# Performance work log

Measured on AMD Instinct MI355X. Metric: run time of the kernel, lower is better.

## Reference

```python
import jax, jax.numpy as jnp
import numpy as np

T = 512      # sequence length
D = 256      # char input dim
H = 512      # hidden dim
E = 256      # word embedding dim
V = 100000   # word alphabet size
KC = 2       # max skip-cells consumed per step
KP = 2       # max words starting per step
M = 340      # total lattice matches


def _build_gaz():
    # Deterministic lattice: at every 3rd position, two matched words of lengths 2 and 4.
    rng = np.random.default_rng(0)
    prod_word = np.zeros((T, KP), np.int32)
    prod_dest = np.full((T, KP), M, np.int32)   # default -> dummy slot
    prod_mask = np.zeros((T, KP), np.int32)
    cons_idx = np.zeros((T, KC), np.int32)
    cons_mask = np.zeros((T, KC), np.int32)
    cnt = np.zeros(T, np.int64)
    m = 0
    for t in range(0, T, 3):
        if t + 3 >= T:
            break
        for k, L in enumerate((2, 4)):
            e = t + L - 1  # end position where this word's cell is consumed
            prod_word[t, k] = rng.integers(0, V)
            prod_dest[t, k] = m
            prod_mask[t, k] = 1
            cons_idx[e, cnt[e]] = m
            cons_mask[e, cnt[e]] = 1
            cnt[e] += 1
            m += 1
    assert m == M
    return prod_word, prod_dest, prod_mask, cons_idx, cons_mask


def setup_inputs() -> dict:
    key = jax.random.key(0)
    ks = jax.random.split(key, 10)
    pw, pd, pm, ci, cm = _build_gaz()
    s = jnp.float32(0.05)
    return {
        "x": jax.random.normal(ks[0], (1, T, D), jnp.float32),
        "emb": jax.random.normal(ks[1], (V, E), jnp.float32) * s,
        "weight_ih": jax.random.normal(ks[2], (D, 3 * H), jnp.float32) * s,
        "weight_hh": jax.random.normal(ks[3], (H, 3 * H), jnp.float32) * s,
        "bias": jnp.zeros((3 * H,), jnp.float32),
        "alpha_weight_ih": jax.random.normal(ks[4], (D, H), jnp.float32) * s,
        "alpha_weight_hh": jax.random.normal(ks[5], (H, H), jnp.float32) * s,
        "alpha_bias": jnp.zeros((H,), jnp.float32),
        "w_weight_ih": jax.random.normal(ks[6], (E, 3 * H), jnp.float32) * s,
        "w_weight_hh": jax.random.normal(ks[7], (H, 3 * H), jnp.float32) * s,
        "w_bias": jnp.zeros((3 * H,), jnp.float32),
        "prod_word": jnp.asarray(pw),
        "prod_dest": jnp.asarray(pd),
        "prod_mask": jnp.asarray(pm),
        "cons_idx": jnp.asarray(ci),
        "cons_mask": jnp.asarray(cm),
        "num_matches": M,
    }


def _lattice_forward(x, emb, Wih, Whh, b, aWih, aWhh, ab, wWih, wWhh, wb,
                     prod_word, prod_dest, prod_mask, cons_idx, cons_mask, num_matches):
    Hd = Whh.shape[0]
    seq = jnp.transpose(x, (1, 0, 2))            # (T, 1, D) -- batch=1 as in original
    store0 = jnp.zeros((num_matches + 1, Hd), x.dtype)  # global skip-word cell store (+dummy)
    h0 = jnp.zeros((1, Hd), x.dtype)
    c0 = jnp.zeros((1, Hd), x.dtype)
    cmaskf = cons_mask.astype(x.dtype)           # (T, KC)
    pdest = jnp.where(prod_mask.astype(bool), prod_dest, num_matches)  # padded -> dummy slot

    def step(carry, inp):
        h, c, store = carry
        xt, cidx, cm, pw, pd = inp               # xt: (1,D)
        # MultiInputLSTMCell
        gates = xt @ Wih + h @ Whh + b           # (1, 3H)
        i, o, g = jnp.split(gates, 3, axis=1)
        i = jax.nn.sigmoid(i)
        o = jax.nn.sigmoid(o)
        g = jnp.tanh(g)
        c_in = store[cidx]                       # (KC, H) skip-word cell states ending here
        alpha = jnp.exp(jax.nn.sigmoid(xt @ aWih + ab + c_in @ aWhh)) * cm[:, None]
        ei = jnp.exp(i)                          # exp-normalize over [i; alpha] as in original
        denom = ei + alpha.sum(0, keepdims=True)
        c_skip = (g * ei + (c_in * alpha).sum(0, keepdims=True)) / denom
        c_plain = (1.0 - i) * c + i * g          # c_num == 0 branch
        c1 = jnp.where(cm.sum() > 0, c_skip, c_plain)
        h1 = o * jnp.tanh(c1)
        # WordLSTMCell for words starting at this position (dropout is identity in eval)
        we = emb[pw]                             # (KP, E)
        wg = we @ wWih + h1 @ wWhh + wb          # (KP, 3H)
        f2, i2, g2 = jnp.split(wg, 3, axis=1)
        ct = jax.nn.sigmoid(f2) * c1 + jax.nn.sigmoid(i2) * jnp.tanh(g2)  # (KP, H)
        store = store.at[pd].set(ct)             # padded rows write to dummy slot
        return (h1, c1, store), (h1[0], c1[0])

    (_, _, _), (hs, cs) = jax.lax.scan(
        step, (h0, c0, store0), (seq, cons_idx, cmaskf, prod_word, pdest))
    return hs[None], cs[None]                    # (1, T, H) each, like unsqueeze(0)


def reference(x, emb, weight_ih, weight_hh, bias, alpha_weight_ih, alpha_weight_hh,
              alpha_bias, w_weight_ih, w_weight_hh, w_bias,
              prod_word, prod_dest, prod_mask, cons_idx, cons_mask, num_matches):
    return _lattice_forward(x, emb, weight_ih, weight_hh, bias,
                            alpha_weight_ih, alpha_weight_hh, alpha_bias,
                            w_weight_ih, w_weight_hh, w_bias,
                            prod_word, prod_dest, prod_mask, cons_idx, cons_mask,
                            num_matches)
```

## Files before the change

### kernel.cpp

```cpp
#include <hip/hip_runtime.h>
#include <stdint.h>


#define T_LEN 512
#define H_DIM 512
#define G3    1536
#define NWG   32
#define NT    256
#define CH    16
#define SENTU 0xFFFFFFFFu
#define WDOG  (1 << 17)
#define SCOPE_AGENT __HIP_MEMORY_SCOPE_AGENT

typedef unsigned u32x4v __attribute__((ext_vector_type(4)));

__device__ __forceinline__ float sigf(float x) { return 1.0f / (1.0f + __expf(-x)); }
__device__ __forceinline__ float tanhfast(float x) {
  x = fminf(fmaxf(x, -15.f), 15.f);
  float t = __expf(2.f * x);
  return (t - 1.f) / (t + 1.f);
}

__device__ __forceinline__ void mload16x2(const float* p0, const float* p1,
                                          u32x4v& a, u32x4v& b) {
  asm volatile("global_load_dwordx4 %0, %2, off sc1\n\t"
               "global_load_dwordx4 %1, %3, off sc1\n\t"
               "s_waitcnt vmcnt(0)"
               : "=&v"(a), "=&v"(b) : "v"(p0), "v"(p1) : "memory");
}
__device__ __forceinline__ bool sent4(u32x4v v) {
  return v.x == SENTU || v.y == SENTU || v.z == SENTU || v.w == SENTU;
}

#define REP32(F) F(0) F(1) F(2) F(3) F(4) F(5) F(6) F(7) F(8) F(9) F(10) F(11) \
                 F(12) F(13) F(14) F(15) F(16) F(17) F(18) F(19) F(20) F(21) F(22) \
                 F(23) F(24) F(25) F(26) F(27) F(28) F(29) F(30) F(31)

#define DECLW(u) float4 wA##u = {0.f,0.f,0.f,0.f}, wB##u = {0.f,0.f,0.f,0.f};

#define LDA1(u) wA##u = make_float4(srcA[(size_t)(ks4 + u*16 + 0) * ldA + gA],  \
                                    srcA[(size_t)(ks4 + u*16 + 1) * ldA + gA],  \
                                    srcA[(size_t)(ks4 + u*16 + 2) * ldA + gA],  \
                                    srcA[(size_t)(ks4 + u*16 + 3) * ldA + gA]);
#define LDB1(u) wB##u = make_float4(srcB[(size_t)(ks4 + u*16 + 0) * (size_t)G3 + gA], \
                                    srcB[(size_t)(ks4 + u*16 + 1) * (size_t)G3 + gA], \
                                    srcB[(size_t)(ks4 + u*16 + 2) * (size_t)G3 + gA], \
                                    srcB[(size_t)(ks4 + u*16 + 3) * (size_t)G3 + gA]);

#define DOTA1(u) { float4 hv = *(const float4*)&vecp[ks4 + u*16];                \
                   q.x += hv.x*wA##u.x; q.y += hv.y*wA##u.y;                     \
                   q.z += hv.z*wA##u.z; q.w += hv.w*wA##u.w; }
#define DOTB1(u) { float4 hv = *(const float4*)&vecp[ks4 + u*16];                \
                   q.x += hv.x*wB##u.x; q.y += hv.y*wB##u.y;                     \
                   q.z += hv.z*wB##u.z; q.w += hv.w*wB##u.w; }
#define DOT_FIN(dst, g) { float acc = (q.x + q.y) + (q.z + q.w);                 \
                          acc += __shfl_down(acc, 2); acc += __shfl_down(acc, 1);\
                          if (((g) & 3) == 0) dst = acc; }

#define STAGE16(k)  do {                                                         \
    const float* row_ = store + (size_t)l_ci[e * 2 + (k)] * H_DIM;               \
    u32x4v r0_, r1_;                                                             \
    int gd_ = 0;                                                                 \
    do { mload16x2(row_ + lane * 4, row_ + 256 + lane * 4, r0_, r1_); }          \
    while ((sent4(r0_) || sent4(r1_)) && ++gd_ < WDOG);                          \
    *(u32x4v*)&cins[par][k][lane * 4] = r0_;                                     \
    *(u32x4v*)&cins[par][k][256 + lane * 4] = r1_;                               \
  } while (0)

#define ALPHA_DOT(k)  do {                                                       \
    if (l_cm[e * 2 + (k)]) {                                                     \
      asm volatile("s_waitcnt lgkmcnt(0)" ::: "memory");                         \
      __builtin_amdgcn_sched_barrier(0);                                         \
      const float* vecp = &cins[par][k][0];                                      \
      float4 q = {0.f, 0.f, 0.f, 0.f};                                           \
      REP32(DOTA1)                                                               \
      DOT_FIN(ds_a[(k) * CH + dcol], lane)                                       \
    }                                                                            \
  } while (0)

__global__ __launch_bounds__(256) void proj_fused(
    const float* __restrict__ x, const float* __restrict__ Wih, const float* __restrict__ bias,
    const float* __restrict__ aWih, const float* __restrict__ ab,
    const float* __restrict__ emb, const float* __restrict__ wWih, const float* __restrict__ wb,
    const int* __restrict__ prod_word,
    float* __restrict__ Xg, float* __restrict__ Xa, float* __restrict__ Wgx) {
  const int b = blockIdx.x;
  const float *A, *W, *bi;
  float* out;
  const int* gather = nullptr;
  int rt, N, cb;
  if (b < 96)       { A = x;   W = Wih;  bi = bias; out = Xg;  N = 1536; rt = (b / 6) * 32;        cb = (b % 6) * 256; }
  else if (b < 128) { int bb = b - 96;  A = x;   W = aWih; bi = ab; out = Xa;  N = 512;  rt = (bb / 2) * 32; cb = (bb % 2) * 256; }
  else              { int bb = b - 128; A = emb; W = wWih; bi = wb; out = Wgx; N = 1536; gather = prod_word; rt = (bb / 6) * 32; cb = (bb % 6) * 256; }
  __shared__ float As[32][256];
  const int tid = threadIdx.x;
  for (int rr = 0; rr < 32; ++rr) {
    int r = rt + rr;
    int src = gather ? gather[r] : r;
    As[rr][tid] = A[(long)src * 256 + tid];
  }
  __syncthreads();
  const int c = cb + tid;
  float acc[32];
#pragma unroll
  for (int rr = 0; rr < 32; ++rr) acc[rr] = 0.f;
#pragma unroll 4
  for (int k = 0; k < 256; ++k) {
    float wv = W[(long)k * N + c];
#pragma unroll
    for (int rr = 0; rr < 32; ++rr) acc[rr] += As[rr][k] * wv;
  }
  float bv = bi[c];
  for (int rr = 0; rr < 32; ++rr) out[(long)(rt + rr) * N + c] = acc[rr] + bv;
}

__global__ __attribute__((amdgpu_flat_work_group_size(NT, NT), amdgpu_waves_per_eu(1, 1)))
void lattice_seq(
    const float* __restrict__ Whh, const float* __restrict__ aWhh, const float* __restrict__ wWhh,
    const float* __restrict__ Xg, const float* __restrict__ Xa, const float* __restrict__ Wgx,
    const int* __restrict__ prod_mask, const int* __restrict__ prod_dest,
    const int* __restrict__ cons_idx,  const int* __restrict__ cons_mask,
    float* __restrict__ Hbuf,
    float* __restrict__ store,
    float* __restrict__ out)
{
  const int tid = threadIdx.x;
  const int w = blockIdx.x;
  const int j0 = w * CH;
  float* outh = out;
  float* outc = out + (size_t)T_LEN * H_DIM;

  __shared__ float h1s[H_DIM];
  __shared__ float prevc1[CH];
  __shared__ float ds_g[3 * CH];
  __shared__ float ds_wg[3 * CH];
  __shared__ float ds_a[2 * CH];
  __shared__ float cins[2][2][H_DIM];
  __shared__ int l_pm[T_LEN * 2], l_pd[T_LEN * 2], l_ci[T_LEN * 2], l_cm[T_LEN * 2];

  for (int i = tid; i < T_LEN * 2; i += NT) {
    l_pm[i] = prod_mask[i];
    l_pd[i] = prod_dest[i];
    l_ci[i] = cons_idx[i];
    l_cm[i] = cons_mask[i];
  }

  int dcol, ks4;
  if (tid < 192) { dcol = tid >> 2; ks4 = (tid & 3) << 2; }
  else { int lane = tid - 192; dcol = lane >> 2; ks4 = (lane & 3) << 2; }

  REP32(DECLW)
  if (tid < 192) {
    const float* srcA = Whh;
    const float* srcB = wWhh;
    const size_t ldA = G3;
    const int gA = (dcol >> 4) * 512 + j0 + (dcol & 15);
    REP32(LDA1)
    REP32(LDB1)
  } else {
    const float* srcA = aWhh;
    const size_t ldA = H_DIM;
    const int gA = j0 + dcol;
    REP32(LDA1)
  }

  ((float2*)h1s)[tid] = make_float2(0.f, 0.f);
  if (tid < CH) prevc1[tid] = 0.f;
  __syncthreads();

  for (int e = 0; e < T_LEN; ++e) {
    const int p = e - 1;
    const bool prodp = (p >= 0) && ((l_pm[p * 2] | l_pm[p * 2 + 1]) != 0);
    const bool conse = (l_cm[e * 2] | l_cm[e * 2 + 1]) != 0;
    const int par = e & 1;

    bool fresh0 = false, fresh1 = false;
    if (conse && prodp) {
      int m0 = l_ci[e * 2], m1 = l_ci[e * 2 + 1];
      fresh0 = (l_pm[p * 2] && l_pd[p * 2] == m0) || (l_pm[p * 2 + 1] && l_pd[p * 2 + 1] == m0);
      fresh1 = (l_pm[p * 2] && l_pd[p * 2] == m1) || (l_pm[p * 2 + 1] && l_pd[p * 2 + 1] == m1);
    }

    float xg0 = 0, xg1 = 0, xg2 = 0, xa0 = 0;
    if (tid < 16) {
      int j = j0 + tid;
      xg0 = Xg[(size_t)e * G3 + j];
      xg1 = Xg[(size_t)e * G3 + 512 + j];
      xg2 = Xg[(size_t)e * G3 + 1024 + j];
      xa0 = Xa[(size_t)e * H_DIM + j];
    }

    float wg0 = 0, wg1 = 0, wg2 = 0;
    if (tid >= 192) {
      const int lane = tid - 192;
      if (prodp && lane < 32) {
        int k = lane >> 4, jj = lane & 15, r = p * 2 + k;
        wg0 = Wgx[(size_t)r * G3 + j0 + jj];
        wg1 = Wgx[(size_t)r * G3 + 512 + j0 + jj];
        wg2 = Wgx[(size_t)r * G3 + 1024 + j0 + jj];
      }
      if (conse) {
        if (l_cm[e * 2] && !fresh0) STAGE16(0);
        if (l_cm[e * 2 + 1] && !fresh1) STAGE16(1);
      }
      if (e > 0) {
        const float* hrow = Hbuf + (size_t)p * H_DIM;
        u32x4v a, b;
        int gd = 0;
        do { mload16x2(hrow + lane * 4, hrow + 256 + lane * 4, a, b); }
        while ((sent4(a) || sent4(b)) && ++gd < WDOG);
        *(u32x4v*)&h1s[lane * 4] = a;
        *(u32x4v*)&h1s[256 + lane * 4] = b;
      }
    }
    __syncthreads();

    if (prodp) {
      if (tid < 192) {
        const float* vecp = h1s;
        float4 q = {0.f, 0.f, 0.f, 0.f};
        REP32(DOTB1)
        DOT_FIN(ds_wg[dcol], tid)
      }
      __syncthreads();
      if (tid < 192) {
        const float* vecp = h1s;
        float4 q = {0.f, 0.f, 0.f, 0.f};
        REP32(DOTA1)
        DOT_FIN(ds_g[dcol], tid)
      } else {
        const int lane = tid - 192;
        if (lane < 32) {
          int k = lane >> 4, jj = lane & 15, r = p * 2 + k;
          if (l_pm[r]) {
            float f2 = wg0 + ds_wg[jj];
            float i2 = wg1 + ds_wg[16 + jj];
            float g2 = wg2 + ds_wg[32 + jj];
            float ct = sigf(f2) * prevc1[jj] + sigf(i2) * tanhfast(g2);
            __hip_atomic_store(&store[(size_t)l_pd[r] * H_DIM + j0 + jj], ct,
                               __ATOMIC_RELAXED, SCOPE_AGENT);
          }
        }
      }
      __syncthreads();
      if (conse && tid >= 192) {
        const int lane = tid - 192;
        if (l_cm[e * 2] && fresh0) STAGE16(0);
        if (l_cm[e * 2 + 1] && fresh1) STAGE16(1);
        ALPHA_DOT(0);
        ALPHA_DOT(1);
      }
      __syncthreads();
    } else {
      if (tid < 192) {
        const float* vecp = h1s;
        float4 q = {0.f, 0.f, 0.f, 0.f};
        REP32(DOTA1)
        DOT_FIN(ds_g[dcol], tid)
      } else if (conse) {
        const int lane = tid - 192;
        ALPHA_DOT(0);
        ALPHA_DOT(1);
      }
      __syncthreads();
    }

    if (tid < 16) {
      int j = j0 + tid;
      float ipre = xg0 + ds_g[tid];
      float opre = xg1 + ds_g[16 + tid];
      float gpre = xg2 + ds_g[32 + tid];
      float iv = sigf(ipre), ov = sigf(opre), gv = tanhfast(gpre);
      float c1;
      if (conse) {
        float ei = __expf(iv);
        float asum = ei, csum = gv * ei;
#pragma unroll
        for (int k = 0; k < 2; ++k) {
          if (l_cm[e * 2 + k]) {
            float apre = xa0 + ds_a[k * CH + tid];
            float al = __expf(sigf(apre));
            asum += al;
            csum += cins[par][k][j] * al;
          }
        }
        c1 = csum / asum;
      } else {
        c1 = (1.f - iv) * prevc1[tid] + iv * gv;
      }
      float h1 = ov * tanhfast(c1);
      prevc1[tid] = c1;
      __hip_atomic_store(&Hbuf[(size_t)e * H_DIM + j], h1, __ATOMIC_RELAXED, SCOPE_AGENT);
      outh[(size_t)e * H_DIM + j] = h1;
      outc[(size_t)e * H_DIM + j] = c1;
    }
  }
}

extern "C" void kernel_launch(void* const* d_in, const int* in_sizes, int n_in,
                              void* d_out, int out_size, void* d_ws, size_t ws_size,
                              hipStream_t stream) {
  const float* x    = (const float*)d_in[0];
  const float* emb  = (const float*)d_in[1];
  const float* Wih  = (const float*)d_in[2];
  const float* Whh  = (const float*)d_in[3];
  const float* bias = (const float*)d_in[4];
  const float* aWih = (const float*)d_in[5];
  const float* aWhh = (const float*)d_in[6];
  const float* ab   = (const float*)d_in[7];
  const float* wWih = (const float*)d_in[8];
  const float* wWhh = (const float*)d_in[9];
  const float* wb   = (const float*)d_in[10];
  const int* prod_word = (const int*)d_in[11];
  const int* prod_dest = (const int*)d_in[12];
  const int* prod_mask = (const int*)d_in[13];
  const int* cons_idx  = (const int*)d_in[14];
  const int* cons_mask = (const int*)d_in[15];

  float* ws    = (float*)d_ws;
  float* Xg    = ws;
  float* Xa    = Xg + 512 * 1536;
  float* Wgx   = Xa + 512 * 512;
  float* Hbuf  = Wgx + 1024 * 1536;
  float* store = Hbuf + 512 * 512;
  size_t need = ((size_t)512 * 1536 + 512 * 512 + 1024 * 1536 + 512 * 512 + 341 * 512) * 4;
  if (ws_size < need) return;

  hipMemsetAsync(Hbuf, 0xFF, (512 * 512 + 341 * 512) * sizeof(float), stream);

  proj_fused<<<dim3(320), dim3(256), 0, stream>>>(
      x, Wih, bias, aWih, ab, emb, wWih, wb, prod_word, Xg, Xa, Wgx);

  lattice_seq<<<dim3(NWG), dim3(NT), 0, stream>>>(
      Whh, aWhh, wWhh, Xg, Xa, Wgx,
      prod_mask, prod_dest, cons_idx, cons_mask,
      Hbuf, store, (float*)d_out);
}
```

Before: 1.956 ms.

## Fuse projection GEMM into persistent recurrent kernel with sentinel-polled dataflow

Merges the input-projection kernel into the sequential lattice kernel. Extra workgroups compute Xg/Xa/Wgx and publish them with agent-scope stores. The recurrent workgroups poll those buffers for the sentinel value before use, so the recurrence can start before all projections finish and one kernel launch is saved. The memset now also sentinel-fills the whole workspace, which adds memset traffic. The change relies on the 32 recurrent blocks being co-resident with the projection blocks, and projection blocks with the 1-wave occupancy attribute may contend with the recurrent blocks for CUs. Store staging was also reordered so non-fresh cell rows are fetched after the h row.

```diff
diff --git a/kernel.cpp b/kernel.cpp
--- a/kernel.cpp
+++ b/kernel.cpp
@@ -6,6 +6,7 @@
 #define H_DIM 512
 #define G3    1536
 #define NWG   32
+#define NPRJ  320
 #define NT    256
 #define CH    16
 #define SENTU 0xFFFFFFFFu
@@ -31,6 +32,33 @@
 __device__ __forceinline__ bool sent4(u32x4v v) {
   return v.x == SENTU || v.y == SENTU || v.z == SENTU || v.w == SENTU;
 }
+
+#define POLL4(v0, v1, v2, v3, p0, p1, p2, p3, need) do {                         \
+    int gd_ = 0; bool ok_;                                                       \
+    do {                                                                         \
+      asm volatile("global_load_dword %0, %4, off sc1\n\t"                       \
+                   "global_load_dword %1, %5, off sc1\n\t"                       \
+                   "global_load_dword %2, %6, off sc1\n\t"                       \
+                   "global_load_dword %3, %7, off sc1\n\t"                       \
+                   "s_waitcnt vmcnt(0)"                                          \
+                   : "=&v"(v0), "=&v"(v1), "=&v"(v2), "=&v"(v3)                  \
+                   : "v"(p0), "v"(p1), "v"(p2), "v"(p3) : "memory");             \
+      ok_ = !(need) || (v0 != SENTU && v1 != SENTU && v2 != SENTU && v3 != SENTU);\
+    } while (!__all(ok_) && ++gd_ < WDOG);                                       \
+  } while (0)
+
+#define POLL3(v0, v1, v2, p0, p1, p2, need) do {                                 \
+    int gd_ = 0; bool ok_;                                                       \
+    do {                                                                         \
+      asm volatile("global_load_dword %0, %3, off sc1\n\t"                       \
+                   "global_load_dword %1, %4, off sc1\n\t"                       \
+                   "global_load_dword %2, %5, off sc1\n\t"                       \
+                   "s_waitcnt vmcnt(0)"                                          \
+                   : "=&v"(v0), "=&v"(v1), "=&v"(v2)                             \
+                   : "v"(p0), "v"(p1), "v"(p2) : "memory");                      \
+      ok_ = !(need) || (v0 != SENTU && v1 != SENTU && v2 != SENTU);              \
+    } while (!__all(ok_) && ++gd_ < WDOG);                                       \
+  } while (0)
 
 #define REP32(F) F(0) F(1) F(2) F(3) F(4) F(5) F(6) F(7) F(8) F(9) F(10) F(11) \
                  F(12) F(13) F(14) F(15) F(16) F(17) F(18) F(19) F(20) F(21) F(22) \
@@ -56,16 +84,6 @@
 #define DOT_FIN(dst, g) { float acc = (q.x + q.y) + (q.z + q.w);                 \
                           acc += __shfl_down(acc, 2); acc += __shfl_down(acc, 1);\
                           if (((g) & 3) == 0) dst = acc; }
-
-#define STAGE16(k)  do {                                                         \
-    const float* row_ = store + (size_t)l_ci[e * 2 + (k)] * H_DIM;               \
-    u32x4v r0_, r1_;                                                             \
-    int gd_ = 0;                                                                 \
-    do { mload16x2(row_ + lane * 4, row_ + 256 + lane * 4, r0_, r1_); }          \
-    while ((sent4(r0_) || sent4(r1_)) && ++gd_ < WDOG);                          \
-    *(u32x4v*)&cins[par][k][lane * 4] = r0_;                                     \
-    *(u32x4v*)&cins[par][k][256 + lane * 4] = r1_;                               \
-  } while (0)
 
 #define ALPHA_DOT(k)  do {                                                       \
     if (l_cm[e * 2 + (k)]) {                                                     \
@@ -78,58 +96,27 @@
     }                                                                            \
   } while (0)
 
-__global__ __launch_bounds__(256) void proj_fused(
-    const float* __restrict__ x, const float* __restrict__ Wih, const float* __restrict__ bias,
+__global__ __attribute__((amdgpu_flat_work_group_size(NT, NT), amdgpu_waves_per_eu(1, 1)))
+void fused_all(
+    const float* __restrict__ x,
+    const float* __restrict__ emb,
+    const float* __restrict__ Wih, const float* __restrict__ bias,
     const float* __restrict__ aWih, const float* __restrict__ ab,
-    const float* __restrict__ emb, const float* __restrict__ wWih, const float* __restrict__ wb,
-    const int* __restrict__ prod_word,
-    float* __restrict__ Xg, float* __restrict__ Xa, float* __restrict__ Wgx) {
-  const int b = blockIdx.x;
-  const float *A, *W, *bi;
-  float* out;
-  const int* gather = nullptr;
-  int rt, N, cb;
-  if (b < 96)       { A = x;   W = Wih;  bi = bias; out = Xg;  N = 1536; rt = (b / 6) * 32;        cb = (b % 6) * 256; }
-  else if (b < 128) { int bb = b - 96;  A = x;   W = aWih; bi = ab; out = Xa;  N = 512;  rt = (bb / 2) * 32; cb = (bb % 2) * 256; }
-  else              { int bb = b - 128; A = emb; W = wWih; bi = wb; out = Wgx; N = 1536; gather = prod_word; rt = (bb / 6) * 32; cb = (bb % 6) * 256; }
-  __shared__ float As[32][256];
-  const int tid = threadIdx.x;
-  for (int rr = 0; rr < 32; ++rr) {
-    int r = rt + rr;
-    int src = gather ? gather[r] : r;
-    As[rr][tid] = A[(long)src * 256 + tid];
-  }
-  __syncthreads();
-  const int c = cb + tid;
-  float acc[32];
-#pragma unroll
-  for (int rr = 0; rr < 32; ++rr) acc[rr] = 0.f;
-#pragma unroll 4
-  for (int k = 0; k < 256; ++k) {
-    float wv = W[(long)k * N + c];
-#pragma unroll
-    for (int rr = 0; rr < 32; ++rr) acc[rr] += As[rr][k] * wv;
-  }
-  float bv = bi[c];
-  for (int rr = 0; rr < 32; ++rr) out[(long)(rt + rr) * N + c] = acc[rr] + bv;
-}
-
-__global__ __attribute__((amdgpu_flat_work_group_size(NT, NT), amdgpu_waves_per_eu(1, 1)))
-void lattice_seq(
+    const float* __restrict__ wWih, const float* __restrict__ wb,
     const float* __restrict__ Whh, const float* __restrict__ aWhh, const float* __restrict__ wWhh,
-    const float* __restrict__ Xg, const float* __restrict__ Xa, const float* __restrict__ Wgx,
-    const int* __restrict__ prod_mask, const int* __restrict__ prod_dest,
-    const int* __restrict__ cons_idx,  const int* __restrict__ cons_mask,
+    const int* __restrict__ prod_word, const int* __restrict__ prod_mask,
+    const int* __restrict__ prod_dest, const int* __restrict__ cons_idx,
+    const int* __restrict__ cons_mask,
+    float* __restrict__ Xg,
+    float* __restrict__ Xa,
+    float* __restrict__ Wgx,
     float* __restrict__ Hbuf,
     float* __restrict__ store,
     float* __restrict__ out)
 {
   const int tid = threadIdx.x;
-  const int w = blockIdx.x;
-  const int j0 = w * CH;
-  float* outh = out;
-  float* outc = out + (size_t)T_LEN * H_DIM;
-
+
+  __shared__ float As[32][256];
   __shared__ float h1s[H_DIM];
   __shared__ float prevc1[CH];
   __shared__ float ds_g[3 * CH];
@@ -137,6 +124,43 @@
   __shared__ float ds_a[2 * CH];
   __shared__ float cins[2][2][H_DIM];
   __shared__ int l_pm[T_LEN * 2], l_pd[T_LEN * 2], l_ci[T_LEN * 2], l_cm[T_LEN * 2];
+
+  if (blockIdx.x >= NWG) {
+    const int b = blockIdx.x - NWG;
+    const float *A, *W, *bi;
+    float* o;
+    const int* gather = nullptr;
+    int rt, N, cb;
+    if (b < 96)       { A = x;   W = Wih;  bi = bias; o = Xg;  N = 1536; rt = (b / 6) * 32;        cb = (b % 6) * 256; }
+    else if (b < 128) { int bb = b - 96;  A = x;   W = aWih; bi = ab; o = Xa;  N = 512;  rt = (bb / 2) * 32; cb = (bb % 2) * 256; }
+    else              { int bb = b - 128; A = emb; W = wWih; bi = wb; o = Wgx; N = 1536; gather = prod_word; rt = (bb / 6) * 32; cb = (bb % 6) * 256; }
+    for (int rr = 0; rr < 32; ++rr) {
+      int r = rt + rr;
+      int src = gather ? gather[r] : r;
+      As[rr][tid] = A[(size_t)src * 256 + tid];
+    }
+    __syncthreads();
+    const int c = cb + tid;
+    float acc[32];
+#pragma unroll
+    for (int rr = 0; rr < 32; ++rr) acc[rr] = 0.f;
+#pragma unroll 4
+    for (int k = 0; k < 256; ++k) {
+      float wv = W[(size_t)k * N + c];
+#pragma unroll
+      for (int rr = 0; rr < 32; ++rr) acc[rr] += As[rr][k] * wv;
+    }
+    float bv = bi[c];
+    for (int rr = 0; rr < 32; ++rr)
+      __hip_atomic_store(&o[(size_t)(rt + rr) * N + c], acc[rr] + bv,
+                         __ATOMIC_RELAXED, SCOPE_AGENT);
+    return;
+  }
+
+  const int w = blockIdx.x;
+  const int j0 = w * CH;
+  float* outh = out;
+  float* outc = out + (size_t)T_LEN * H_DIM;
 
   for (int i = tid; i < T_LEN * 2; i += NT) {
     l_pm[i] = prod_mask[i];
@@ -182,26 +206,25 @@
     }
 
     float xg0 = 0, xg1 = 0, xg2 = 0, xa0 = 0;
-    if (tid < 16) {
-      int j = j0 + tid;
-      xg0 = Xg[(size_t)e * G3 + j];
-      xg1 = Xg[(size_t)e * G3 + 512 + j];
-      xg2 = Xg[(size_t)e * G3 + 1024 + j];
-      xa0 = Xa[(size_t)e * H_DIM + j];
+    if (tid < 64) {
+      const int jj = tid & 15;
+      const float* pXg = Xg + (size_t)e * G3 + j0 + jj;
+      const float* pXa = Xa + (size_t)e * H_DIM + j0 + jj;
+      unsigned v0, v1, v2, v3;
+      POLL4(v0, v1, v2, v3, pXg, pXg + 512, pXg + 1024, pXa, tid < 16);
+      xg0 = __uint_as_float(v0);
+      xg1 = __uint_as_float(v1);
+      xg2 = __uint_as_float(v2);
+      xa0 = __uint_as_float(v3);
     }
 
     float wg0 = 0, wg1 = 0, wg2 = 0;
     if (tid >= 192) {
       const int lane = tid - 192;
-      if (prodp && lane < 32) {
-        int k = lane >> 4, jj = lane & 15, r = p * 2 + k;
-        wg0 = Wgx[(size_t)r * G3 + j0 + jj];
-        wg1 = Wgx[(size_t)r * G3 + 512 + j0 + jj];
-        wg2 = Wgx[(size_t)r * G3 + 1024 + j0 + jj];
-      }
+      int sA = -1, sB = -1;
       if (conse) {
-        if (l_cm[e * 2] && !fresh0) STAGE16(0);
-        if (l_cm[e * 2 + 1] && !fresh1) STAGE16(1);
+        if (l_cm[e * 2] && !fresh0) sA = 0;
+        if (l_cm[e * 2 + 1] && !fresh1) { if (sA < 0) sA = 1; else sB = 1; }
       }
       if (e > 0) {
         const float* hrow = Hbuf + (size_t)p * H_DIM;
@@ -211,6 +234,31 @@
         while ((sent4(a) || sent4(b)) && ++gd < WDOG);
         *(u32x4v*)&h1s[lane * 4] = a;
         *(u32x4v*)&h1s[256 + lane * 4] = b;
+      }
+      for (int k = 0; k < 2; ++k) {
+        int sk = (k == 0) ? sA : sB;
+        if (sk >= 0) {
+          const float* srow = store + (size_t)l_ci[e * 2 + sk] * H_DIM;
+          u32x4v s0, s1;
+          int gd = 0;
+          do { mload16x2(srow + lane * 4, srow + 256 + lane * 4, s0, s1); }
+          while ((sent4(s0) || sent4(s1)) && ++gd < WDOG);
+          *(u32x4v*)&cins[par][sk][lane * 4] = s0;
+          *(u32x4v*)&cins[par][sk][256 + lane * 4] = s1;
+        }
+      }
+      if (prodp && lane < 32) {
+        int k = lane >> 4, jj = lane & 15, r = p * 2 + k;
+        const float* pW = Wgx + (size_t)r * G3 + j0 + jj;
+        unsigned v0, v1, v2;
+        POLL3(v0, v1, v2, pW, pW + 512, pW + 1024, lane < 32);
+        wg0 = __uint_as_float(v0);
+        wg1 = __uint_as_float(v1);
+        wg2 = __uint_as_float(v2);
+      } else if (prodp) {
+        unsigned v0, v1, v2;
+        const float* pW = Wgx + (size_t)(p * 2) * G3 + j0;
+        POLL3(v0, v1, v2, pW, pW + 512, pW + 1024, false);
       }
     }
     __syncthreads();
@@ -245,8 +293,18 @@
       __syncthreads();
       if (conse && tid >= 192) {
         const int lane = tid - 192;
-        if (l_cm[e * 2] && fresh0) STAGE16(0);
-        if (l_cm[e * 2 + 1] && fresh1) STAGE16(1);
+        for (int k = 0; k < 2; ++k) {
+          bool fr = (k == 0) ? fresh0 : fresh1;
+          if (l_cm[e * 2 + k] && fr) {
+            const float* srow = store + (size_t)l_ci[e * 2 + k] * H_DIM;
+            u32x4v s0, s1;
+            int gd = 0;
+            do { mload16x2(srow + lane * 4, srow + 256 + lane * 4, s0, s1); }
+            while ((sent4(s0) || sent4(s1)) && ++gd < WDOG);
+            *(u32x4v*)&cins[par][k][lane * 4] = s0;
+            *(u32x4v*)&cins[par][k][256 + lane * 4] = s1;
+          }
+        }
         ALPHA_DOT(0);
         ALPHA_DOT(1);
       }
@@ -323,16 +381,14 @@
   float* Wgx   = Xa + 512 * 512;
   float* Hbuf  = Wgx + 1024 * 1536;
   float* store = Hbuf + 512 * 512;
-  size_t need = ((size_t)512 * 1536 + 512 * 512 + 1024 * 1536 + 512 * 512 + 341 * 512) * 4;
-  if (ws_size < need) return;
-
-  hipMemsetAsync(Hbuf, 0xFF, (512 * 512 + 341 * 512) * sizeof(float), stream);
-
-  proj_fused<<<dim3(320), dim3(256), 0, stream>>>(
-      x, Wih, bias, aWih, ab, emb, wWih, wb, prod_word, Xg, Xa, Wgx);
-
-  lattice_seq<<<dim3(NWG), dim3(NT), 0, stream>>>(
-      Whh, aWhh, wWhh, Xg, Xa, Wgx,
-      prod_mask, prod_dest, cons_idx, cons_mask,
-      Hbuf, store, (float*)d_out);
-}
+  size_t nfl = (size_t)512 * 1536 + 512 * 512 + 1024 * 1536 + 512 * 512 + 341 * 512;
+  if (ws_size < nfl * 4) return;
+
+  hipMemsetAsync(Xg, 0xFF, nfl * sizeof(float), stream);
+
+  fused_all<<<dim3(NWG + NPRJ), dim3(NT), 0, stream>>>(
+      x, emb, Wih, bias, aWih, ab, wWih, wb,
+      Whh, aWhh, wWhh,
+      prod_word, prod_mask, prod_dest, cons_idx, cons_mask,
+      Xg, Xa, Wgx, Hbuf, store, (float*)d_out);
+}
```

Result: slower. 2.153 ms (+10.0%).
